# Optimization experiments

Measured on AMD Instinct MI355X. Metric: run time of the kernel, lower is better.

Reference implementation:

```python
import jax, jax.numpy as jnp
import numpy as np

B, INPUT_DIM, EMB_DIM = 16384, 2048, 768
DOMAIN_NUM, MEMORY_NUM, TAU = 9, 10, 32.0


def setup_inputs() -> dict:
    key = jax.random.key(0)
    k1, k2, k3, k4, k5 = jax.random.split(key, 5)
    feature = jax.random.normal(k1, (B, INPUT_DIM), dtype=jnp.float32)
    category = jax.random.randint(k2, (B,), 0, DOMAIN_NUM, dtype=jnp.int64)
    # Linear(input_dim, emb_dim, bias=False) weights: [emb_dim, input_dim]
    W_topic = jax.random.normal(k3, (EMB_DIM, INPUT_DIM), dtype=jnp.float32) * 0.02
    W_domain = jax.random.normal(k4, (EMB_DIM, INPUT_DIM), dtype=jnp.float32) * 0.02
    # domain_num Embedding(memory_num, emb_dim) tables, stacked: [D, M, E]
    memory_tables = jax.random.normal(k5, (DOMAIN_NUM, MEMORY_NUM, EMB_DIM), dtype=jnp.float32)
    return {"feature": feature, "W_topic": W_topic, "W_domain": W_domain,
            "memory_tables": memory_tables, "category": category}


def reference(feature, W_topic, W_domain, memory_tables, category):
    eps = 1e-12
    # F.normalize(feature, p=2, dim=-1)
    norm = jnp.maximum(jnp.linalg.norm(feature, axis=-1, keepdims=True), eps)
    feat = feature / norm                                   # [B, I]
    # per-sample gather of each sample's category memory table: [B, M, E]
    mem = memory_tables[category]
    # faithful quirk: loop over domain_num indexes the BATCH dim of the stack
    D = memory_tables.shape[0]
    mems_d = mem[:D]                                        # [D, M, E]
    t = feat @ W_topic.T                                    # [B, E]
    topic_att = jax.nn.softmax(jnp.einsum('be,dme->bdm', t, mems_d) * TAU, axis=-1)
    sep = jnp.einsum('bdm,dme->bde', topic_att, mems_d)     # [B, D, E]
    dproj = feat @ W_domain.T                               # [B, E]
    domain_att = jax.nn.softmax(jnp.einsum('bde,be->bd', sep, dproj) * TAU, axis=-1)
    return domain_att[:, None, :]                           # [B, 1, D]
```

## Files before the change

### kernel.cpp

```cpp
#include <hip/hip_runtime.h>
#include <math.h>

#define TAU_F 32.0f

typedef __attribute__((ext_vector_type(8))) _Float16 half8;
typedef __attribute__((ext_vector_type(2))) __fp16 half2v;
typedef __attribute__((ext_vector_type(4))) float f32x4;

union HU { uint4 u; half8 v; };

__global__ __launch_bounds__(256) void gproj2(
    const float* __restrict__ Wt, const float* __restrict__ Wd,
    const float* __restrict__ mem, const int* __restrict__ cat,
    float* __restrict__ P)
{
    __shared__ float Ml[96 * 36];
    __shared__ float Wl[32 * 68];

    const int bid = blockIdx.x;
    const int mat = bid >> 7;
    const int ks  = (bid >> 5) & 3;
    const int ct  = bid & 31;
    const int c0  = ct * 64;
    const int tid = threadIdx.x;
    const float* __restrict__ W = mat ? Wd : Wt;

    const int tr = tid >> 4;
    const int tc = tid & 15;

    float acc[6][4];
    #pragma unroll
    for (int j = 0; j < 6; ++j)
        #pragma unroll
        for (int q = 0; q < 4; ++q) acc[j][q] = 0.f;

    for (int ch = 0; ch < 6; ++ch) {
        __syncthreads();
        #pragma unroll
        for (int p = 0; p < 3; ++p) {
            const int idx = tid + 256 * p;
            const int r   = idx >> 3;
            const int kq  = idx & 7;
            float4 v = make_float4(0.f, 0.f, 0.f, 0.f);
            if (r < 90) {
                const int d = r / 10;
                const int mrow = cat[d] * 10 + (r - d * 10);
                v = *(const float4*)(mem + (size_t)mrow * 768 + ks * 192 + ch * 32 + kq * 4);
            }
            *(float4*)(Ml + r * 36 + kq * 4) = v;
        }
        #pragma unroll
        for (int p = 0; p < 2; ++p) {
            const int idx = tid + 256 * p;
            const int e   = idx >> 4;
            const int c4  = (idx & 15) * 4;
            *(float4*)(Wl + e * 68 + c4) =
                *(const float4*)(W + (size_t)(ks * 192 + ch * 32 + e) * 2048 + c0 + c4);
        }
        __syncthreads();

        #pragma unroll
        for (int e = 0; e < 32; e += 4) {
            float4 m4[6], w4[4];
            #pragma unroll
            for (int j = 0; j < 6; ++j) m4[j] = *(const float4*)(Ml + (tr * 6 + j) * 36 + e);
            #pragma unroll
            for (int q = 0; q < 4; ++q) w4[q] = *(const float4*)(Wl + (e + q) * 68 + tc * 4);
            #pragma unroll
            for (int j = 0; j < 6; ++j) {
                const float mv[4] = {m4[j].x, m4[j].y, m4[j].z, m4[j].w};
                #pragma unroll
                for (int q = 0; q < 4; ++q) {
                    acc[j][0] = fmaf(mv[q], w4[q].x, acc[j][0]);
                    acc[j][1] = fmaf(mv[q], w4[q].y, acc[j][1]);
                    acc[j][2] = fmaf(mv[q], w4[q].z, acc[j][2]);
                    acc[j][3] = fmaf(mv[q], w4[q].w, acc[j][3]);
                }
            }
        }
    }

    #pragma unroll
    for (int j = 0; j < 6; ++j) {
        float4 v = make_float4(acc[j][0], acc[j][1], acc[j][2], acc[j][3]);
        *(float4*)(P + (size_t)ks * 393216 + (size_t)(mat * 96 + tr * 6 + j) * 2048 + c0 + tc * 4) = v;
    }
}

__global__ __launch_bounds__(256) void split_g3(
    const float* __restrict__ P, unsigned short* __restrict__ gB)
{
    const int u  = blockIdx.x * 256 + threadIdx.x;
    const int n  = u >> 8;
    const int k0 = (u & 255) * 8;

    float s[8] = {0.f, 0.f, 0.f, 0.f, 0.f, 0.f, 0.f, 0.f};
    #pragma unroll
    for (int ks = 0; ks < 4; ++ks) {
        const float4 a = *(const float4*)(P + (size_t)ks * 393216 + (size_t)n * 2048 + k0);
        const float4 b = *(const float4*)(P + (size_t)ks * 393216 + (size_t)n * 2048 + k0 + 4);
        s[0] += a.x; s[1] += a.y; s[2] += a.z; s[3] += a.w;
        s[4] += b.x; s[5] += b.y; s[6] += b.z; s[7] += b.w;
    }
    union { _Float16 h[8]; uint4 u4; } hi, lo;
    #pragma unroll
    for (int e = 0; e < 8; ++e) {
        const _Float16 h = (_Float16)s[e];
        hi.h[e] = h;
        lo.h[e] = (_Float16)(s[e] - (float)h);
    }
    const int kc = k0 >> 5;
    const int lq = (k0 >> 3) & 3;
    const int nq = n / 48;
    const int rm = n - nq * 48;
    const int j  = rm >> 4;
    const int lm = rm & 15;
    const size_t fH = (size_t)((kc * 12 + nq * 3 + j) * 2 + 0) * 512 + lq * 128 + lm * 8;
    const size_t fL = (size_t)((kc * 12 + nq * 3 + j) * 2 + 1) * 512 + lq * 128 + lm * 8;
    *(uint4*)(gB + fH) = hi.u4;
    *(uint4*)(gB + fL) = lo.u4;
}

__global__ __launch_bounds__(256, 2) void fused_mfma4(
    const float* __restrict__ feat, const unsigned short* __restrict__ gB,
    float* __restrict__ P2, float* __restrict__ ssqp)
{
    __shared__ __align__(16) unsigned short aS[20480];

    const int tid = threadIdx.x;
    const int rt  = blockIdx.x >> 2;
    const int ks  = blockIdx.x & 3;
    const int row0 = rt * 128;

    const int w  = tid >> 6, l = tid & 63;
    const int lm = l & 15,  lq = l >> 4;
    const int r8 = tid >> 3, kq = tid & 7;

    f32x4 acc[8][3];
    #pragma unroll
    for (int i = 0; i < 8; ++i)
        #pragma unroll
        for (int j = 0; j < 3; ++j) acc[i][j] = (f32x4)0.f;
    float ssq4[4] = {0.f, 0.f, 0.f, 0.f};

    const float* fbase = feat + (size_t)(row0 + r8) * 2048 + ks * 512 + kq * 4;
    const unsigned short* bbase = gB + (size_t)ks * 196608 + (w * 3) * 1024 + l * 8;

    float4 fa[4], fan[4];
    #pragma unroll
    for (int p = 0; p < 4; ++p) fa[p] = *(const float4*)(fbase + p * 65536);
    uint4 bh0[3], bl0[3], bh1[3], bl1[3];
    #pragma unroll
    for (int j = 0; j < 3; ++j) {
        bh0[j] = *(const uint4*)(bbase + j * 1024);
        bl0[j] = *(const uint4*)(bbase + j * 1024 + 512);
        bh1[j] = *(const uint4*)(bbase + 12288 + j * 1024);
        bl1[j] = *(const uint4*)(bbase + 12288 + j * 1024 + 512);
    }
    #pragma unroll
    for (int p = 0; p < 4; ++p) {
        const float4 v = fa[p];
        ssq4[p] = fmaf(v.x, v.x, ssq4[p]); ssq4[p] = fmaf(v.y, v.y, ssq4[p]);
        ssq4[p] = fmaf(v.z, v.z, ssq4[p]); ssq4[p] = fmaf(v.w, v.w, ssq4[p]);
        half2v h01 = __builtin_amdgcn_cvt_pkrtz(v.x, v.y);
        half2v h23 = __builtin_amdgcn_cvt_pkrtz(v.z, v.w);
        half2v l01 = __builtin_amdgcn_cvt_pkrtz(v.x - (float)h01[0], v.y - (float)h01[1]);
        half2v l23 = __builtin_amdgcn_cvt_pkrtz(v.z - (float)h23[0], v.w - (float)h23[1]);
        union { half2v h2[2]; uint2 u2; } uh, ul;
        uh.h2[0] = h01; uh.h2[1] = h23;
        ul.h2[0] = l01; ul.h2[1] = l23;
        const int row = p * 32 + r8;
        *(uint2*)(aS + 0 * 5120 + row * 40 + kq * 4) = uh.u2;
        *(uint2*)(aS + 1 * 5120 + row * 40 + kq * 4) = ul.u2;
    }
    #pragma unroll
    for (int p = 0; p < 4; ++p) fan[p] = *(const float4*)(fbase + 32 + p * 65536);
    __syncthreads();

    #pragma unroll 2
    for (int kc = 0; kc < 16; ++kc) {
        const int kn = (kc + 2 < 16) ? kc + 2 : 15;
        float4 fa2[4];
        #pragma unroll
        for (int p = 0; p < 4; ++p) fa2[p] = *(const float4*)(fbase + kn * 32 + p * 65536);
        uint4 bh2[3], bl2[3];
        #pragma unroll
        for (int j = 0; j < 3; ++j) {
            bh2[j] = *(const uint4*)(bbase + (size_t)kn * 12288 + j * 1024);
            bl2[j] = *(const uint4*)(bbase + (size_t)kn * 12288 + j * 1024 + 512);
        }

        if (kc < 15) {
            const int nb = (kc + 1) & 1;
            #pragma unroll
            for (int p = 0; p < 4; ++p) {
                const float4 v = fan[p];
                ssq4[p] = fmaf(v.x, v.x, ssq4[p]); ssq4[p] = fmaf(v.y, v.y, ssq4[p]);
                ssq4[p] = fmaf(v.z, v.z, ssq4[p]); ssq4[p] = fmaf(v.w, v.w, ssq4[p]);
                half2v h01 = __builtin_amdgcn_cvt_pkrtz(v.x, v.y);
                half2v h23 = __builtin_amdgcn_cvt_pkrtz(v.z, v.w);
                half2v l01 = __builtin_amdgcn_cvt_pkrtz(v.x - (float)h01[0], v.y - (float)h01[1]);
                half2v l23 = __builtin_amdgcn_cvt_pkrtz(v.z - (float)h23[0], v.w - (float)h23[1]);
                union { half2v h2[2]; uint2 u2; } uh, ul;
                uh.h2[0] = h01; uh.h2[1] = h23;
                ul.h2[0] = l01; ul.h2[1] = l23;
                const int row = p * 32 + r8;
                *(uint2*)(aS + (nb * 2 + 0) * 5120 + row * 40 + kq * 4) = uh.u2;
                *(uint2*)(aS + (nb * 2 + 1) * 5120 + row * 40 + kq * 4) = ul.u2;
            }
        }

        const int cb = kc & 1;
        const unsigned short* aH = aS + (cb * 2 + 0) * 5120;
        const unsigned short* aL = aS + (cb * 2 + 1) * 5120;
        #pragma unroll
        for (int ih = 0; ih < 2; ++ih) {
            half8 fh[4], fl[4];
            #pragma unroll
            for (int i2 = 0; i2 < 4; ++i2) {
                const int row = (ih * 4 + i2) * 16 + lm;
                HU th, tl;
                th.u = *(const uint4*)(aH + row * 40 + lq * 8);
                tl.u = *(const uint4*)(aL + row * 40 + lq * 8);
                fh[i2] = th.v; fl[i2] = tl.v;
            }
            #pragma unroll
            for (int j = 0; j < 3; ++j) {
                HU h8, l8; h8.u = bh0[j]; l8.u = bl0[j];
                #pragma unroll
                for (int i2 = 0; i2 < 4; ++i2) {
                    const int i = ih * 4 + i2;
                    acc[i][j] = __builtin_amdgcn_mfma_f32_16x16x32_f16(fh[i2], h8.v, acc[i][j], 0, 0, 0);
                    acc[i][j] = __builtin_amdgcn_mfma_f32_16x16x32_f16(fh[i2], l8.v, acc[i][j], 0, 0, 0);
                    acc[i][j] = __builtin_amdgcn_mfma_f32_16x16x32_f16(fl[i2], h8.v, acc[i][j], 0, 0, 0);
                }
            }
        }
        __syncthreads();

        #pragma unroll
        for (int p = 0; p < 4; ++p) fan[p] = fa2[p];
        #pragma unroll
        for (int j = 0; j < 3; ++j) {
            bh0[j] = bh1[j]; bl0[j] = bl1[j];
            bh1[j] = bh2[j]; bl1[j] = bl2[j];
        }
    }

    #pragma unroll
    for (int p = 0; p < 4; ++p) {
        float s = ssq4[p];
        s += __shfl_xor(s, 1, 64);
        s += __shfl_xor(s, 2, 64);
        s += __shfl_xor(s, 4, 64);
        if ((tid & 7) == 0) ssqp[(size_t)ks * 16384 + row0 + p * 32 + r8] = s;
    }

    #pragma unroll
    for (int i = 0; i < 8; ++i)
        #pragma unroll
        for (int j = 0; j < 3; ++j)
            #pragma unroll
            for (int r = 0; r < 4; ++r)
                P2[((size_t)ks * 16384 + row0 + i * 16 + lq * 4 + r) * 192 + w * 48 + j * 16 + lm]
                    = acc[i][j][r];
}

#define EP_SPAD 196
__global__ __launch_bounds__(256) void ep_kernel(
    const float* __restrict__ P2, const float* __restrict__ ssqp,
    float* __restrict__ out)
{
    __shared__ float sc[64 * EP_SPAD];
    const int tid  = threadIdx.x;
    const int row0 = blockIdx.x * 64;

    float4 s[12];
    #pragma unroll
    for (int p = 0; p < 12; ++p) s[p] = make_float4(0.f, 0.f, 0.f, 0.f);
    #pragma unroll
    for (int ks = 0; ks < 4; ++ks)
        #pragma unroll
        for (int p = 0; p < 12; ++p) {
            const int u   = p * 256 + tid;
            const int row = u / 48;
            const int c4  = (u - row * 48) * 4;
            const float4 v = *(const float4*)(P2 + ((size_t)ks * 16384 + row0 + row) * 192 + c4);
            s[p].x += v.x; s[p].y += v.y; s[p].z += v.z; s[p].w += v.w;
        }
    #pragma unroll
    for (int p = 0; p < 12; ++p) {
        const int u   = p * 256 + tid;
        const int row = u / 48;
        const int c4  = (u - row * 48) * 4;
        *(float4*)(sc + row * EP_SPAD + c4) = s[p];
    }
    float nsq = 0.f;
    if (tid < 64) {
        nsq = ssqp[row0 + tid] + ssqp[16384 + row0 + tid]
            + ssqp[32768 + row0 + tid] + ssqp[49152 + row0 + tid];
    }
    __syncthreads();

    if (tid < 64) {
        const int r = tid;
        const float inv = TAU_F / fmaxf(sqrtf(nsq), 1e-12f);
        const float* scr = sc + (size_t)r * EP_SPAD;
        float lg[9];
        float dmax = -1e30f;
        #pragma unroll
        for (int d = 0; d < 9; ++d) {
            const float* v = scr + d * 10;
            const float* u = scr + 96 + d * 10;
            float mx = v[0];
            #pragma unroll
            for (int m = 1; m < 10; ++m) mx = fmaxf(mx, v[m]);
            float ssum = 0.f, dot = 0.f;
            #pragma unroll
            for (int m = 0; m < 10; ++m) {
                const float p = __expf((v[m] - mx) * inv);
                ssum += p;
                dot = fmaf(p, u[m], dot);
            }
            const float lgt = (dot / ssum) * inv;
            lg[d] = lgt;
            dmax = fmaxf(dmax, lgt);
        }
        float s2 = 0.f;
        #pragma unroll
        for (int d = 0; d < 9; ++d) { const float p = __expf(lg[d] - dmax); lg[d] = p; s2 += p; }
        const float r2 = 1.0f / s2;
        #pragma unroll
        for (int d = 0; d < 9; ++d)
            out[(size_t)(row0 + r) * 9 + d] = lg[d] * r2;
    }
}

extern "C" void kernel_launch(void* const* d_in, const int* in_sizes, int n_in,
                              void* d_out, int out_size, void* d_ws, size_t ws_size,
                              hipStream_t stream) {
    const float* feature = (const float*)d_in[0];
    const float* Wt      = (const float*)d_in[1];
    const float* Wd      = (const float*)d_in[2];
    const float* mem     = (const float*)d_in[3];
    const int*   cat     = (const int*)d_in[4];

    float* P2 = (float*)d_ws;
    float* P  = (float*)d_ws;
    unsigned short* gB = (unsigned short*)((char*)d_ws + 50331648);
    float* ssqp = (float*)((char*)d_ws + 50331648 + 1572864);
    float* out = (float*)d_out;

    gproj2<<<256, 256, 0, stream>>>(Wt, Wd, mem, cat, P);
    split_g3<<<192, 256, 0, stream>>>(P, gB);
    fused_mfma4<<<512, 256, 0, stream>>>(feature, gB, P2, ssqp);
    ep_kernel<<<256, 256, 0, stream>>>(P2, ssqp, out);
}
```

Before: 251.1 us.

## Retile main MFMA kernel to 64-row tiles with 2-way K split

Reworks the fused GEMM kernel so each block covers 64 rows and half of K (two K-splits instead of four), with smaller accumulators, a single-stage B register prefetch and half the LDS footprint. Launch bounds now allow three blocks per SM. The epilogue sums two partials instead of four. This cuts the partial-result traffic written to and read back from the workspace and raises occupancy. In exchange, each B fragment loaded from global memory is reused across fewer rows, and the shallower prefetch can expose more load latency.

```diff
diff --git a/kernel.cpp b/kernel.cpp
--- a/kernel.cpp
+++ b/kernel.cpp
@@ -121,148 +121,124 @@
     *(uint4*)(gB + fL) = lo.u4;
 }
 
-__global__ __launch_bounds__(256, 2) void fused_mfma4(
+__global__ __launch_bounds__(256, 3) void fused_mfma5(
     const float* __restrict__ feat, const unsigned short* __restrict__ gB,
     float* __restrict__ P2, float* __restrict__ ssqp)
 {
-    __shared__ __align__(16) unsigned short aS[20480];
+    __shared__ __align__(16) unsigned short aS[10240];
 
     const int tid = threadIdx.x;
-    const int rt  = blockIdx.x >> 2;
-    const int ks  = blockIdx.x & 3;
-    const int row0 = rt * 128;
-
-    const int w  = tid >> 6, l = tid & 63;
+    const int rt  = blockIdx.x >> 1;
+    const int ks  = blockIdx.x & 1;
+    const int row0 = rt * 64;
+
+    const int nq = tid >> 6, l = tid & 63;
     const int lm = l & 15,  lq = l >> 4;
-    const int r8 = tid >> 3, kq = tid & 7;
-
-    f32x4 acc[8][3];
-    #pragma unroll
-    for (int i = 0; i < 8; ++i)
+    const int r8 = tid >> 2, kq = tid & 3;
+
+    f32x4 acc[4][3];
+    #pragma unroll
+    for (int i = 0; i < 4; ++i)
         #pragma unroll
         for (int j = 0; j < 3; ++j) acc[i][j] = (f32x4)0.f;
-    float ssq4[4] = {0.f, 0.f, 0.f, 0.f};
-
-    const float* fbase = feat + (size_t)(row0 + r8) * 2048 + ks * 512 + kq * 4;
-    const unsigned short* bbase = gB + (size_t)ks * 196608 + (w * 3) * 1024 + l * 8;
-
-    float4 fa[4], fan[4];
-    #pragma unroll
-    for (int p = 0; p < 4; ++p) fa[p] = *(const float4*)(fbase + p * 65536);
-    uint4 bh0[3], bl0[3], bh1[3], bl1[3];
+    float ssq = 0.f;
+
+    const float* fbase = feat + (size_t)(row0 + r8) * 2048 + ks * 1024 + kq * 8;
+    const unsigned short* bbase = gB + (size_t)ks * 393216 + (nq * 3) * 1024 + l * 8;
+
+    float4 f0 = *(const float4*)(fbase);
+    float4 f1 = *(const float4*)(fbase + 4);
+    uint4 bh[3], bl[3];
     #pragma unroll
     for (int j = 0; j < 3; ++j) {
-        bh0[j] = *(const uint4*)(bbase + j * 1024);
-        bl0[j] = *(const uint4*)(bbase + j * 1024 + 512);
-        bh1[j] = *(const uint4*)(bbase + 12288 + j * 1024);
-        bl1[j] = *(const uint4*)(bbase + 12288 + j * 1024 + 512);
-    }
-    #pragma unroll
-    for (int p = 0; p < 4; ++p) {
-        const float4 v = fa[p];
-        ssq4[p] = fmaf(v.x, v.x, ssq4[p]); ssq4[p] = fmaf(v.y, v.y, ssq4[p]);
-        ssq4[p] = fmaf(v.z, v.z, ssq4[p]); ssq4[p] = fmaf(v.w, v.w, ssq4[p]);
-        half2v h01 = __builtin_amdgcn_cvt_pkrtz(v.x, v.y);
-        half2v h23 = __builtin_amdgcn_cvt_pkrtz(v.z, v.w);
-        half2v l01 = __builtin_amdgcn_cvt_pkrtz(v.x - (float)h01[0], v.y - (float)h01[1]);
-        half2v l23 = __builtin_amdgcn_cvt_pkrtz(v.z - (float)h23[0], v.w - (float)h23[1]);
-        union { half2v h2[2]; uint2 u2; } uh, ul;
-        uh.h2[0] = h01; uh.h2[1] = h23;
-        ul.h2[0] = l01; ul.h2[1] = l23;
-        const int row = p * 32 + r8;
-        *(uint2*)(aS + 0 * 5120 + row * 40 + kq * 4) = uh.u2;
-        *(uint2*)(aS + 1 * 5120 + row * 40 + kq * 4) = ul.u2;
-    }
-    #pragma unroll
-    for (int p = 0; p < 4; ++p) fan[p] = *(const float4*)(fbase + 32 + p * 65536);
+        bh[j] = *(const uint4*)(bbase + j * 1024);
+        bl[j] = *(const uint4*)(bbase + j * 1024 + 512);
+    }
+    {
+        const float xs[8] = {f0.x, f0.y, f0.z, f0.w, f1.x, f1.y, f1.z, f1.w};
+        union { half2v h2[4]; uint4 u4; } uh, ul;
+        #pragma unroll
+        for (int e = 0; e < 4; ++e) {
+            const float a = xs[2 * e], b = xs[2 * e + 1];
+            ssq = fmaf(a, a, ssq); ssq = fmaf(b, b, ssq);
+            half2v h = __builtin_amdgcn_cvt_pkrtz(a, b);
+            uh.h2[e] = h;
+            ul.h2[e] = __builtin_amdgcn_cvt_pkrtz(a - (float)h[0], b - (float)h[1]);
+        }
+        *(uint4*)(aS + 0 * 2560 + r8 * 40 + kq * 8) = uh.u4;
+        *(uint4*)(aS + 1 * 2560 + r8 * 40 + kq * 8) = ul.u4;
+    }
+    float4 fn0 = *(const float4*)(fbase + 32);
+    float4 fn1 = *(const float4*)(fbase + 36);
     __syncthreads();
 
-    #pragma unroll 2
-    for (int kc = 0; kc < 16; ++kc) {
-        const int kn = (kc + 2 < 16) ? kc + 2 : 15;
-        float4 fa2[4];
-        #pragma unroll
-        for (int p = 0; p < 4; ++p) fa2[p] = *(const float4*)(fbase + kn * 32 + p * 65536);
-        uint4 bh2[3], bl2[3];
+    for (int kc = 0; kc < 32; ++kc) {
+        const int ka = (kc + 2 < 32) ? kc + 2 : 31;
+        float4 fa0 = *(const float4*)(fbase + ka * 32);
+        float4 fa1 = *(const float4*)(fbase + ka * 32 + 4);
+        const int kb = (kc + 1 < 32) ? kc + 1 : 31;
+        uint4 bhn[3], bln[3];
         #pragma unroll
         for (int j = 0; j < 3; ++j) {
-            bh2[j] = *(const uint4*)(bbase + (size_t)kn * 12288 + j * 1024);
-            bl2[j] = *(const uint4*)(bbase + (size_t)kn * 12288 + j * 1024 + 512);
-        }
-
-        if (kc < 15) {
+            bhn[j] = *(const uint4*)(bbase + (size_t)kb * 12288 + j * 1024);
+            bln[j] = *(const uint4*)(bbase + (size_t)kb * 12288 + j * 1024 + 512);
+        }
+
+        if (kc < 31) {
             const int nb = (kc + 1) & 1;
-            #pragma unroll
-            for (int p = 0; p < 4; ++p) {
-                const float4 v = fan[p];
-                ssq4[p] = fmaf(v.x, v.x, ssq4[p]); ssq4[p] = fmaf(v.y, v.y, ssq4[p]);
-                ssq4[p] = fmaf(v.z, v.z, ssq4[p]); ssq4[p] = fmaf(v.w, v.w, ssq4[p]);
-                half2v h01 = __builtin_amdgcn_cvt_pkrtz(v.x, v.y);
-                half2v h23 = __builtin_amdgcn_cvt_pkrtz(v.z, v.w);
-                half2v l01 = __builtin_amdgcn_cvt_pkrtz(v.x - (float)h01[0], v.y - (float)h01[1]);
-                half2v l23 = __builtin_amdgcn_cvt_pkrtz(v.z - (float)h23[0], v.w - (float)h23[1]);
-                union { half2v h2[2]; uint2 u2; } uh, ul;
-                uh.h2[0] = h01; uh.h2[1] = h23;
-                ul.h2[0] = l01; ul.h2[1] = l23;
-                const int row = p * 32 + r8;
-                *(uint2*)(aS + (nb * 2 + 0) * 5120 + row * 40 + kq * 4) = uh.u2;
-                *(uint2*)(aS + (nb * 2 + 1) * 5120 + row * 40 + kq * 4) = ul.u2;
-            }
+            const float xs[8] = {fn0.x, fn0.y, fn0.z, fn0.w, fn1.x, fn1.y, fn1.z, fn1.w};
+            union { half2v h2[4]; uint4 u4; } uh, ul;
+            #pragma unroll
+            for (int e = 0; e < 4; ++e) {
+                const float a = xs[2 * e], b = xs[2 * e + 1];
+                ssq = fmaf(a, a, ssq); ssq = fmaf(b, b, ssq);
+                half2v h = __builtin_amdgcn_cvt_pkrtz(a, b);
+                uh.h2[e] = h;
+                ul.h2[e] = __builtin_amdgcn_cvt_pkrtz(a - (float)h[0], b - (float)h[1]);
+            }
+            *(uint4*)(aS + (nb * 2 + 0) * 2560 + r8 * 40 + kq * 8) = uh.u4;
+            *(uint4*)(aS + (nb * 2 + 1) * 2560 + r8 * 40 + kq * 8) = ul.u4;
         }
 
         const int cb = kc & 1;
-        const unsigned short* aH = aS + (cb * 2 + 0) * 5120;
-        const unsigned short* aL = aS + (cb * 2 + 1) * 5120;
-        #pragma unroll
-        for (int ih = 0; ih < 2; ++ih) {
-            half8 fh[4], fl[4];
-            #pragma unroll
-            for (int i2 = 0; i2 < 4; ++i2) {
-                const int row = (ih * 4 + i2) * 16 + lm;
-                HU th, tl;
-                th.u = *(const uint4*)(aH + row * 40 + lq * 8);
-                tl.u = *(const uint4*)(aL + row * 40 + lq * 8);
-                fh[i2] = th.v; fl[i2] = tl.v;
-            }
-            #pragma unroll
-            for (int j = 0; j < 3; ++j) {
-                HU h8, l8; h8.u = bh0[j]; l8.u = bl0[j];
-                #pragma unroll
-                for (int i2 = 0; i2 < 4; ++i2) {
-                    const int i = ih * 4 + i2;
-                    acc[i][j] = __builtin_amdgcn_mfma_f32_16x16x32_f16(fh[i2], h8.v, acc[i][j], 0, 0, 0);
-                    acc[i][j] = __builtin_amdgcn_mfma_f32_16x16x32_f16(fh[i2], l8.v, acc[i][j], 0, 0, 0);
-                    acc[i][j] = __builtin_amdgcn_mfma_f32_16x16x32_f16(fl[i2], h8.v, acc[i][j], 0, 0, 0);
-                }
+        const unsigned short* aH = aS + (cb * 2 + 0) * 2560;
+        const unsigned short* aL = aS + (cb * 2 + 1) * 2560;
+        half8 fh[4], fl[4];
+        #pragma unroll
+        for (int i = 0; i < 4; ++i) {
+            HU th, tl;
+            th.u = *(const uint4*)(aH + (i * 16 + lm) * 40 + lq * 8);
+            tl.u = *(const uint4*)(aL + (i * 16 + lm) * 40 + lq * 8);
+            fh[i] = th.v; fl[i] = tl.v;
+        }
+        #pragma unroll
+        for (int j = 0; j < 3; ++j) {
+            HU h8, l8; h8.u = bh[j]; l8.u = bl[j];
+            #pragma unroll
+            for (int i = 0; i < 4; ++i) {
+                acc[i][j] = __builtin_amdgcn_mfma_f32_16x16x32_f16(fh[i], h8.v, acc[i][j], 0, 0, 0);
+                acc[i][j] = __builtin_amdgcn_mfma_f32_16x16x32_f16(fh[i], l8.v, acc[i][j], 0, 0, 0);
+                acc[i][j] = __builtin_amdgcn_mfma_f32_16x16x32_f16(fl[i], h8.v, acc[i][j], 0, 0, 0);
             }
         }
         __syncthreads();
 
-        #pragma unroll
-        for (int p = 0; p < 4; ++p) fan[p] = fa2[p];
-        #pragma unroll
-        for (int j = 0; j < 3; ++j) {
-            bh0[j] = bh1[j]; bl0[j] = bl1[j];
-            bh1[j] = bh2[j]; bl1[j] = bl2[j];
-        }
-    }
-
-    #pragma unroll
-    for (int p = 0; p < 4; ++p) {
-        float s = ssq4[p];
-        s += __shfl_xor(s, 1, 64);
-        s += __shfl_xor(s, 2, 64);
-        s += __shfl_xor(s, 4, 64);
-        if ((tid & 7) == 0) ssqp[(size_t)ks * 16384 + row0 + p * 32 + r8] = s;
-    }
-
-    #pragma unroll
-    for (int i = 0; i < 8; ++i)
+        fn0 = fa0; fn1 = fa1;
+        #pragma unroll
+        for (int j = 0; j < 3; ++j) { bh[j] = bhn[j]; bl[j] = bln[j]; }
+    }
+
+    ssq += __shfl_xor(ssq, 1, 64);
+    ssq += __shfl_xor(ssq, 2, 64);
+    if ((tid & 3) == 0) ssqp[(size_t)ks * 16384 + row0 + (tid >> 2)] = ssq;
+
+    #pragma unroll
+    for (int i = 0; i < 4; ++i)
         #pragma unroll
         for (int j = 0; j < 3; ++j)
             #pragma unroll
             for (int r = 0; r < 4; ++r)
-                P2[((size_t)ks * 16384 + row0 + i * 16 + lq * 4 + r) * 192 + w * 48 + j * 16 + lm]
+                P2[((size_t)ks * 16384 + row0 + i * 16 + lq * 4 + r) * 192 + nq * 48 + j * 16 + lm]
                     = acc[i][j][r];
 }
 
@@ -279,7 +255,7 @@
     #pragma unroll
     for (int p = 0; p < 12; ++p) s[p] = make_float4(0.f, 0.f, 0.f, 0.f);
     #pragma unroll
-    for (int ks = 0; ks < 4; ++ks)
+    for (int ks = 0; ks < 2; ++ks)
         #pragma unroll
         for (int p = 0; p < 12; ++p) {
             const int u   = p * 256 + tid;
@@ -297,8 +273,7 @@
     }
     float nsq = 0.f;
     if (tid < 64) {
-        nsq = ssqp[row0 + tid] + ssqp[16384 + row0 + tid]
-            + ssqp[32768 + row0 + tid] + ssqp[49152 + row0 + tid];
+        nsq = ssqp[row0 + tid] + ssqp[16384 + row0 + tid];
     }
     __syncthreads();
 
@@ -353,6 +328,6 @@
 
     gproj2<<<256, 256, 0, stream>>>(Wt, Wd, mem, cat, P);
     split_g3<<<192, 256, 0, stream>>>(P, gB);
-    fused_mfma4<<<512, 256, 0, stream>>>(feature, gB, P2, ssqp);
+    fused_mfma5<<<512, 256, 0, stream>>>(feature, gB, P2, ssqp);
     ep_kernel<<<256, 256, 0, stream>>>(P2, ssqp, out);
 }
```

New measurement: 257.0 us. 2.4% more time.
